# Optimization experiments

Hardware: AMD Instinct MI355X
Metric: run time of the kernel (lower is better)

Reference implementation:

```python
import jax, jax.numpy as jnp
import numpy as np
from jax import lax

T, B, D_IN, D_DAY, H, D_OUT = 64, 32, 4096, 256, 256, 942


def setup_inputs() -> dict:
    key = jax.random.key(0)
    ks = jax.random.split(key, 18)
    s = 0.05
    def rn(k, shape):
        return jax.random.normal(k, shape, jnp.float32) * s
    return {
        "x": jax.random.uniform(ks[0], (T, B, D_IN), jnp.float32),
        "W_emb": rn(ks[1], (D_DAY, D_IN)), "b_emb": rn(ks[2], (D_DAY,)),
        "Wih_f": rn(ks[3], (3 * H, D_DAY)), "Whh_f": rn(ks[4], (3 * H, H)),
        "bih_f": rn(ks[5], (3 * H,)), "bhh_f": rn(ks[6], (3 * H,)),
        "Wih_r": rn(ks[7], (3 * H, D_DAY)), "Whh_r": rn(ks[8], (3 * H, H)),
        "bih_r": rn(ks[9], (3 * H,)), "bhh_r": rn(ks[10], (3 * H,)),
        "attn_w": rn(ks[11], (2 * H,)), "attn_b": rn(ks[12], ()),
        "W_ao": rn(ks[13], (D_DAY, 4 * H)), "b_ao": rn(ks[14], (D_DAY,)),
        "W_o": rn(ks[15], (D_OUT, D_DAY)), "b_o": rn(ks[16], (D_OUT,)),
    }


def _gru_cell(xt, h, Wih, Whh, bih, bhh):
    # PyTorch nn.GRU cell math
    gi = xt @ Wih.T + bih          # [B, 3H]
    gh = h @ Whh.T + bhh           # [B, 3H]
    ir, iz, inn = jnp.split(gi, 3, axis=-1)
    hr, hz, hn = jnp.split(gh, 3, axis=-1)
    r = jax.nn.sigmoid(ir + hr)
    z = jax.nn.sigmoid(iz + hz)
    n = jnp.tanh(inn + r * hn)
    return (1.0 - z) * n + z * h


def _run_gru(seq, Wih, Whh, bih, bhh):
    # seq: [L, B, D] -> all hidden states [L, B, H], h0 = zeros
    h0 = jnp.zeros((seq.shape[1], H), seq.dtype)
    def step(h, xt):
        h2 = _gru_cell(xt, h, Wih, Whh, bih, bhh)
        return h2, h2
    return lax.scan(step, h0, seq)[1]


def reference(x, W_emb, b_emb, Wih_f, Whh_f, bih_f, bhh_f,
              Wih_r, Whh_r, bih_r, bhh_r, attn_w, attn_b,
              W_ao, b_ao, W_o, b_o):
    day_emb = jnp.einsum('tbi,di->tbd', x, W_emb) + b_emb       # [T,B,Dday]

    # Forward GRU over the prefix [:i+1] equals the first i+1 states of one full run.
    fwd = _run_gru(day_emb, Wih_f, Whh_f, bih_f, bhh_f)          # [T,B,H]

    # Reverse GRU is recomputed per timestep on the flipped prefix (O(T^2)).
    i_idx = jnp.arange(T)
    j_idx = jnp.arange(T)
    gather = jnp.clip(i_idx[:, None] - j_idx[None, :], 0)        # [T,T]
    rev_in = day_emb[gather]                                     # [T,T,B,Dday]; row i, step j = day_emb[i-j]
    rev = jax.vmap(lambda s: _run_gru(s, Wih_r, Whh_r, bih_r, bhh_r))(rev_in)  # [T,T,B,H]

    # Attention scores on concat(fwd, rev) without materializing the 2H concat:
    w_f, w_r = attn_w[:H], attn_w[H:]
    scores = (jnp.einsum('tbh,h->tb', fwd, w_f)[None, :, :]
              + jnp.einsum('itbh,h->itb', rev, w_r) + attn_b)    # [T(i),T(t),B]
    valid = j_idx[None, :] <= i_idx[:, None]                     # t <= i
    scores = jnp.where(valid[:, :, None], scores, -jnp.inf)
    alpha = jax.nn.softmax(scores, axis=1)                       # softmax over prefix time

    counts = (i_idx + 1).astype(day_emb.dtype)[:, None, None]    # mean over i+1 steps
    c_fwd = jnp.einsum('itb,tbh->ibh', alpha, fwd) / counts      # [T,B,H]
    c_rev = jnp.einsum('itb,itbh->ibh', alpha, rev) / counts     # [T,B,H]
    rev_last = rev[i_idx, i_idx]                                 # rnn_h[-1] reverse half, [T,B,H]

    h_t = jnp.concatenate([c_fwd, c_rev, fwd, rev_last], axis=-1)  # [T,B,4H]
    h_t_out = h_t @ W_ao.T + b_ao                                # [T,B,Dday]
    return jax.nn.sigmoid(h_t_out @ W_o.T + b_o)                 # [T,B,D_OUT]
```

## Files before the change

### kernel.cpp

```cpp
#include <hip/hip_runtime.h>
#include <hip/hip_bf16.h>


typedef __bf16 bf16x8 __attribute__((ext_vector_type(8)));
typedef __bf16 bf16x4 __attribute__((ext_vector_type(4)));
typedef float  f32x4  __attribute__((ext_vector_type(4)));
typedef int    int4v  __attribute__((ext_vector_type(4)));

static constexpr float NEG_L2E = -1.442695041f;
static constexpr float TWO_L2E =  2.885390082f;

static constexpr size_t OFF_PK_EMB = 0;
static constexpr size_t OFF_PK_IH  = 2097152;
static constexpr size_t OFF_WQ     = 2883584;
static constexpr size_t OFF_WSC    = 3276800;
static constexpr size_t OFF_PK_AO  = 3670016;
static constexpr size_t OFF_PK_O   = 4194304;
static constexpr size_t OFF_DAY    = 4685824;
static constexpr size_t OFF_GIT    = 5734400;
static constexpr size_t OFF_BC     = 12025856;
static constexpr size_t OFF_REV    = 18317312;
static constexpr size_t OFF_FWD    = 52396032;
static constexpr size_t OFF_HT     = 53444608;
static constexpr size_t OFF_TMP1   = 57638912;
static constexpr size_t OFF_XB     = OFF_REV;

__device__ __forceinline__ float sigf(float x) {
    return __builtin_amdgcn_rcpf(1.f + __expf(-x));
}

#define LDS_BARRIER() asm volatile("s_waitcnt lgkmcnt(0)\n\ts_barrier" ::: "memory")

__global__ __launch_bounds__(256) void pack_misc(
    const float* __restrict__ We,  const float* __restrict__ Wir, const float* __restrict__ Wif,
    const float* __restrict__ Wao, const float* __restrict__ Wo,  const float* __restrict__ x,
    const float* __restrict__ Whr, const float* __restrict__ Whf,
    const float* __restrict__ bih_r, const float* __restrict__ bih_f,
    const float* __restrict__ bhh_r, const float* __restrict__ bhh_f,
    __bf16* pe, __bf16* pi, __bf16* pao, __bf16* po, __bf16* xb,
    signed char* __restrict__ wq, float* __restrict__ wscale, float* __restrict__ bc)
{
    int b = blockIdx.x;
    if (b >= 5048) {
        int rowb = (b - 5048) * 4 + (threadIdx.x >> 6);
        int t = threadIdx.x & 63;
        int dir = (rowb >= 768) ? 1 : 0;
        int n = rowb - dir * 768;
        const float* src = (dir ? Whf : Whr) + (size_t)n * 256;
        float4 wv = ((const float4*)src)[t];
        float m = fmaxf(fmaxf(fabsf(wv.x), fabsf(wv.y)), fmaxf(fabsf(wv.z), fabsf(wv.w)));
#pragma unroll
        for (int off = 32; off > 0; off >>= 1) m = fmaxf(m, __shfl_xor(m, off));
        m = fmaxf(m, 1e-20f);
        float inv = 127.f / m;
        int q0 = (int)__builtin_rintf(wv.x * inv);
        int q1 = (int)__builtin_rintf(wv.y * inv);
        int q2 = (int)__builtin_rintf(wv.z * inv);
        int q3 = (int)__builtin_rintf(wv.w * inv);
        int pk = (q0 & 0xff) | ((q1 & 0xff) << 8) | ((q2 & 0xff) << 16) | ((q3 & 0xff) << 24);
        int dlane = (n & 15) | (((t >> 2) & 3) << 4);
        size_t byte = (size_t)dir * 196608 + ((size_t)(n >> 4) * 4 + (t >> 4)) * 1024
                    + (size_t)dlane * 16 + (t & 3) * 4;
        *(int*)(wq + byte) = pk;
        if (t == 0) {
            float gc = (n < 512) ? NEG_L2E : TWO_L2E;
            wscale[rowb] = m * (1.f / 16129.f) * gc;
            const float* bi = dir ? bih_f : bih_r;
            const float* bh = dir ? bhh_f : bhh_r;
            bc[rowb] = (n < 512) ? (bi[n] + bh[n]) * NEG_L2E : bi[n] * TWO_L2E;
        }
        return;
    }
    if (b >= 952) {
        size_t base = ((size_t)(b - 952) * 256 + threadIdx.x) * 8;
        float4 v0 = *(const float4*)(x + base);
        float4 v1 = *(const float4*)(x + base + 4);
        bf16x8 o;
        o[0]=(__bf16)v0.x; o[1]=(__bf16)v0.y; o[2]=(__bf16)v0.z; o[3]=(__bf16)v0.w;
        o[4]=(__bf16)v1.x; o[5]=(__bf16)v1.y; o[6]=(__bf16)v1.z; o[7]=(__bf16)v1.w;
        *(bf16x8*)(xb + base) = o;
        return;
    }
    const float* src; __bf16* dst; int Nsrc, k32l, b0; bool ih = false;
    if (b < 512)      { src = We;  dst = pe;          Nsrc = 256; k32l = 7; b0 = 0;   }
    else if (b < 608) { src = Wir; dst = pi;          Nsrc = 768; k32l = 3; b0 = 512; ih = true; }
    else if (b < 704) { src = Wif; dst = pi + 196608; Nsrc = 768; k32l = 3; b0 = 608; ih = true; }
    else if (b < 832) { src = Wao; dst = pao;         Nsrc = 256; k32l = 5; b0 = 704; }
    else              { src = Wo;  dst = po;          Nsrc = 942; k32l = 3; b0 = 832; }
    int t8   = (b - b0) * 256 + threadIdx.x;
    int lane = t8 & 63;
    int K32  = 1 << k32l;
    int K    = K32 << 5;
    int ks   = (t8 >> 6) & (K32 - 1);
    int nt   = t8 >> (6 + k32l);
    int n    = nt * 16 + (lane & 15);
    int k0   = ks * 32 + ((lane >> 4) << 3);
    bf16x8 o;
    if (n < Nsrc) {
        const float* sp = src + (size_t)n * K + k0;
        float4 v0 = *(const float4*)sp;
        float4 v1 = *(const float4*)(sp + 4);
        float s = ih ? ((n < 512) ? NEG_L2E : TWO_L2E) : 1.f;
        o[0]=(__bf16)(v0.x*s); o[1]=(__bf16)(v0.y*s); o[2]=(__bf16)(v0.z*s); o[3]=(__bf16)(v0.w*s);
        o[4]=(__bf16)(v1.x*s); o[5]=(__bf16)(v1.y*s); o[6]=(__bf16)(v1.z*s); o[7]=(__bf16)(v1.w*s);
    } else {
#pragma unroll
        for (int q = 0; q < 8; q++) o[q] = (__bf16)0.f;
    }
    *(bf16x8*)(dst + (size_t)t8 * 8) = o;
}

template<int MODE, int KDIM, int NTILES, int CSTRIDE, int NREAL>
__global__ __launch_bounds__(256) void gemm_k(
    const __bf16* __restrict__ Ap, const __bf16* __restrict__ Bp, void* __restrict__ Cp,
    const float* __restrict__ bias)
{
    __shared__ __align__(16) __bf16 As[32][88];
    const int tid = threadIdx.x;
    const int w = tid >> 6, lane = tid & 63, c = lane & 15, quad = lane >> 4;
    const int mb = blockIdx.x, nb = blockIdx.y;
    constexpr int K32 = KDIM / 32;
    constexpr int NK  = KDIM / 64;
    constexpr int NT_W = NTILES / 2;
    const int wrow = w & 1, ncol0 = (w >> 1) * NT_W;

    f32x4 acc[NT_W];
#pragma unroll
    for (int nt = 0; nt < NT_W; nt++) acc[nt] = (f32x4){0.f, 0.f, 0.f, 0.f};

    const int row = tid >> 3, kp = (tid & 7) * 8;
    uint4 pb;
    auto issue  = [&](int kb) { pb = *(const uint4*)(Ap + (size_t)(mb * 32 + row) * KDIM + kb * 64 + kp); };
    auto commit = [&]() { *(uint4*)&As[row][kp] = pb; };

    bf16x8 bcur[2][NT_W], bnxt[2][NT_W];
    auto loadB = [&](int kb, bf16x8 (&dst)[2][NT_W]) {
#pragma unroll
        for (int kk = 0; kk < 2; kk++)
#pragma unroll
            for (int nt = 0; nt < NT_W; nt++)
                dst[kk][nt] = *(const bf16x8*)(Bp +
                    ((size_t)((nb * NTILES + ncol0 + nt) * K32 + kb * 2 + kk) * 64 + lane) * 8);
    };

    issue(0);
    loadB(0, bcur);
    for (int kb = 0; kb < NK; kb++) {
        commit();
        __syncthreads();
        if (kb + 1 < NK) { issue(kb + 1); loadB(kb + 1, bnxt); }
#pragma unroll
        for (int kk = 0; kk < 2; kk++) {
            bf16x8 a = *(const bf16x8*)&As[wrow * 16 + c][kk * 32 + quad * 8];
#pragma unroll
            for (int nt = 0; nt < NT_W; nt++)
                acc[nt] = __builtin_amdgcn_mfma_f32_16x16x32_bf16(a, bcur[kk][nt], acc[nt], 0, 0, 0);
        }
        if (kb + 1 < NK) {
#pragma unroll
            for (int kk = 0; kk < 2; kk++)
#pragma unroll
                for (int nt = 0; nt < NT_W; nt++) bcur[kk][nt] = bnxt[kk][nt];
        }
        __syncthreads();
    }

#pragma unroll
    for (int nt = 0; nt < NT_W; nt++) {
        int n = nb * (NTILES * 16) + (ncol0 + nt) * 16 + c;
        float bv = (n < NREAL) ? bias[n] : 0.f;
#pragma unroll
        for (int r0 = 0; r0 < 4; r0++) {
            int m = mb * 32 + wrow * 16 + quad * 4 + r0;
            float v = acc[nt][r0] + bv;
            if constexpr (MODE == 0) ((__bf16*)Cp)[(size_t)m * CSTRIDE + n] = (__bf16)v;
            else { if (n < NREAL) ((float*)Cp)[(size_t)m * CSTRIDE + n] = sigf(v); }
        }
    }
}

__global__ __launch_bounds__(1024, 4) void gru_recurrent(
    const signed char* __restrict__ wq, const float* __restrict__ wscale,
    const float* __restrict__ bhh_r, const float* __restrict__ bhh_f,
    const __bf16* __restrict__ Gi,
    __bf16* __restrict__ revb, __bf16* __restrict__ fwdb)
{
    __shared__ __align__(16) signed char hbuf[2][4096];
    const int tid = threadIdx.x;
    const int w = tid >> 6, lane = tid & 63, c = lane & 15, quad = lane >> 4;
    const int bid = blockIdx.x;
    const bool isF = (bid < 2);
    const int ia = isF ? 63 : (63 - ((bid - 2) >> 1));
    const int b0 = (bid & 1) << 4;
    const int steps = ia + 1;
    const float* bhh = isF ? bhh_f : bhh_r;
    __bf16* outb = isF ? fwdb : (revb + ((size_t)(ia * (ia + 1) / 2)) * 8192);
    const int dirb = isF ? 768 : 0;

    const int4v* pw = (const int4v*)(wq + (isF ? 196608 : 0));
    int4v bw[3][4];
#pragma unroll
    for (int g = 0; g < 3; g++)
#pragma unroll
        for (int ks = 0; ks < 4; ks++)
            bw[g][ks] = pw[(size_t)((g * 16 + w) * 4 + ks) * 64 + lane];

    const int dq = (w << 4) + (quad << 2);
    f32x4 sc0 = *(const f32x4*)&wscale[dirb + dq];
    f32x4 sc1 = *(const f32x4*)&wscale[dirb + 256 + dq];
    f32x4 sc2 = *(const f32x4*)&wscale[dirb + 512 + dq];
    f32x4 bnv = *(const f32x4*)&bhh[512 + dq];
#pragma unroll
    for (int q = 0; q < 4; q++) bnv[q] *= TWO_L2E;

    float hreg[4] = {0.f, 0.f, 0.f, 0.f};
    ((int*)hbuf)[tid] = 0; ((int*)hbuf)[tid + 1024] = 0;
    __syncthreads();

    const __bf16* grow = Gi + (size_t)((isF ? 0 : ia) * 32 + b0 + c) * 1536 + dirb + dq;
    const long gstep = isF ? (32 * 1536) : -(32 * 1536);
    __bf16* go = outb + (size_t)(b0 + c) * 256 + dq;

    const int wr_off = (w >> 2) * 1024 + ((c + ((w & 3) << 4)) << 4) + (quad << 2);
    const int rd_off = lane << 4;

    bf16x4 gcur[3], gnxt[3];
#pragma unroll
    for (int g = 0; g < 3; g++) gcur[g] = *(const bf16x4*)(grow + g * 256);

    for (int j = 0; j < steps; j++) {
        const int rb = j & 1, wbuf = rb ^ 1;
        const bool more = (j + 1 < steps);

        if (more) {
            grow += gstep;
#pragma unroll
            for (int g = 0; g < 3; g++) gnxt[g] = *(const bf16x4*)(grow + g * 256);
        }

        int4v a0 = {0,0,0,0}, a1 = {0,0,0,0}, a2 = {0,0,0,0};
#pragma unroll
        for (int ks = 0; ks < 4; ks++) {
            int4v av = *(const int4v*)&hbuf[rb][ks * 1024 + rd_off];
            a0 = __builtin_amdgcn_mfma_i32_16x16x64_i8(bw[0][ks], av, a0, 0, 0, 0);
            a1 = __builtin_amdgcn_mfma_i32_16x16x64_i8(bw[1][ks], av, a1, 0, 0, 0);
            a2 = __builtin_amdgcn_mfma_i32_16x16x64_i8(bw[2][ks], av, a2, 0, 0, 0);
        }

        float f[4];
        bf16x4 hb;
#pragma unroll
        for (int r0 = 0; r0 < 4; r0++) {
            float er = __builtin_amdgcn_exp2f(fmaf((float)a0[r0], sc0[r0], (float)gcur[0][r0]));
            float rg = __builtin_amdgcn_rcpf(1.f + er);
            float ez = __builtin_amdgcn_exp2f(fmaf((float)a1[r0], sc1[r0], (float)gcur[1][r0]));
            float zg = __builtin_amdgcn_rcpf(1.f + ez);
            float narg = fmaf(rg, fmaf((float)a2[r0], sc2[r0], bnv[r0]), (float)gcur[2][r0]);
            float en = __builtin_amdgcn_exp2f(narg);
            float ng = fmaf(-2.f, __builtin_amdgcn_rcpf(1.f + en), 1.f);
            float h  = fmaf(zg, hreg[r0] - ng, ng);
            hreg[r0] = h;
            hb[r0] = (__bf16)h;
            f[r0] = fmaf(h, 127.f, 12582912.f);
        }
        unsigned lo = __builtin_amdgcn_perm(__float_as_uint(f[1]), __float_as_uint(f[0]), 0x00000400u);
        unsigned hi = __builtin_amdgcn_perm(__float_as_uint(f[3]), __float_as_uint(f[2]), 0x04000000u);
        int pk = (int)__builtin_amdgcn_perm(hi, lo, 0x07060100u);

        *(int*)&hbuf[wbuf][wr_off] = pk;
        *(bf16x4*)go = hb;
        go += 8192;
        LDS_BARRIER();
        if (more) {
#pragma unroll
            for (int g = 0; g < 3; g++) gcur[g] = gnxt[g];
        }
    }
}

__global__ __launch_bounds__(512) void attn_kernel(
    const __bf16* __restrict__ revb, const __bf16* __restrict__ fwdb,
    const float* __restrict__ attn_w, const float* __restrict__ attn_bp,
    __bf16* __restrict__ ht)
{
    const int tid = threadIdx.x;
    const int w = tid >> 6, lane = tid & 63;
    const int wid = blockIdx.x * 8 + w;
    const int i = wid >> 5, b = wid & 31;
    const int d0 = lane * 4;

    float wf[4], wr[4];
#pragma unroll
    for (int q = 0; q < 4; q++) { wf[q] = attn_w[d0 + q]; wr[q] = attn_w[256 + d0 + q]; }
    const float ab = attn_bp[0];
    const __bf16* rp = revb + ((size_t)(i * (i + 1) / 2)) * 8192 + (size_t)b * 256 + d0;
    const __bf16* fp = fwdb + (size_t)b * 256 + d0;

    float mx = -1e30f, l = 0.f;
    float cf[4] = {0,0,0,0}, cr[4] = {0,0,0,0};
    bf16x4 rn = *(const bf16x4*)rp, fn = *(const bf16x4*)fp;
    for (int t = 0; t <= i; t++) {
        bf16x4 rv4 = rn, fv4 = fn;
        if (t < i) {
            rn = *(const bf16x4*)(rp + (size_t)(t + 1) * 8192);
            fn = *(const bf16x4*)(fp + (size_t)(t + 1) * 8192);
        }
        float rv[4], fv[4], s = 0.f;
#pragma unroll
        for (int q = 0; q < 4; q++) {
            rv[q] = (float)rv4[q]; fv[q] = (float)fv4[q];
            s += rv[q] * wr[q] + fv[q] * wf[q];
        }
#pragma unroll
        for (int off = 32; off > 0; off >>= 1) s += __shfl_xor(s, off);
        s += ab;
        float mn = fmaxf(mx, s);
        float scl = __expf(mx - mn);
        float p  = __expf(s - mn);
        l = l * scl + p;
#pragma unroll
        for (int q = 0; q < 4; q++) { cf[q] = cf[q] * scl + p * fv[q]; cr[q] = cr[q] * scl + p * rv[q]; }
        mx = mn;
    }
    float inv = __builtin_amdgcn_rcpf(l * (float)(i + 1));
    __bf16* hp = ht + (size_t)(i * 32 + b) * 1024 + d0;
    const __bf16* fl = fp + (size_t)i * 8192;
    const __bf16* rl = rp + (size_t)i * 8192;
#pragma unroll
    for (int q = 0; q < 4; q++) {
        hp[q]       = (__bf16)(cf[q] * inv);
        hp[256 + q] = (__bf16)(cr[q] * inv);
        hp[512 + q] = fl[q];
        hp[768 + q] = rl[q];
    }
}

extern "C" void kernel_launch(void* const* d_in, const int* in_sizes, int n_in,
                              void* d_out, int out_size, void* d_ws, size_t ws_size,
                              hipStream_t stream) {
    const float* x      = (const float*)d_in[0];
    const float* W_emb  = (const float*)d_in[1];
    const float* b_emb  = (const float*)d_in[2];
    const float* Wih_f  = (const float*)d_in[3];
    const float* Whh_f  = (const float*)d_in[4];
    const float* bih_f  = (const float*)d_in[5];
    const float* bhh_f  = (const float*)d_in[6];
    const float* Wih_r  = (const float*)d_in[7];
    const float* Whh_r  = (const float*)d_in[8];
    const float* bih_r  = (const float*)d_in[9];
    const float* bhh_r  = (const float*)d_in[10];
    const float* attn_w = (const float*)d_in[11];
    const float* attn_b = (const float*)d_in[12];
    const float* W_ao   = (const float*)d_in[13];
    const float* b_ao   = (const float*)d_in[14];
    const float* W_o    = (const float*)d_in[15];
    const float* b_o    = (const float*)d_in[16];
    float* out = (float*)d_out;

    char* ws = (char*)d_ws;
    __bf16* pk_emb = (__bf16*)(ws + OFF_PK_EMB);
    __bf16* pk_ih  = (__bf16*)(ws + OFF_PK_IH);
    signed char* wq = (signed char*)(ws + OFF_WQ);
    float*  wsc    = (float*)(ws + OFF_WSC);
    __bf16* pk_ao  = (__bf16*)(ws + OFF_PK_AO);
    __bf16* pk_o   = (__bf16*)(ws + OFF_PK_O);
    __bf16* day    = (__bf16*)(ws + OFF_DAY);
    __bf16* Gi     = (__bf16*)(ws + OFF_GIT);
    float*  bc     = (float*)(ws + OFF_BC);
    __bf16* revb   = (__bf16*)(ws + OFF_REV);
    __bf16* fwdb   = (__bf16*)(ws + OFF_FWD);
    __bf16* ht     = (__bf16*)(ws + OFF_HT);
    __bf16* tmp1   = (__bf16*)(ws + OFF_TMP1);
    __bf16* xb     = (__bf16*)(ws + OFF_XB);

    pack_misc<<<5432, 256, 0, stream>>>(W_emb, Wih_r, Wih_f, W_ao, W_o, x,
                                        Whh_r, Whh_f, bih_r, bih_f, bhh_r, bhh_f,
                                        pk_emb, pk_ih, pk_ao, pk_o, xb, wq, wsc, bc);

    gemm_k<0, 4096, 4, 256, 256><<<dim3(64, 4), 256, 0, stream>>>(xb, pk_emb, day, b_emb);
    gemm_k<0, 256, 4, 1536, 1536><<<dim3(64, 24), 256, 0, stream>>>(day, pk_ih, Gi, bc);

    gru_recurrent<<<130, 1024, 0, stream>>>(wq, wsc, bhh_r, bhh_f, Gi, revb, fwdb);

    attn_kernel<<<256, 512, 0, stream>>>(revb, fwdb, attn_w, attn_b, ht);

    gemm_k<0, 1024, 4, 256, 256><<<dim3(64, 4), 256, 0, stream>>>(ht, pk_ao, tmp1, b_ao);
    gemm_k<1, 256, 4, 942, 942><<<dim3(64, 15), 256, 0, stream>>>(tmp1, pk_o, out, b_o);
}
```

Before: 330.1 us.

## Halve GRU recurrent block size with two M-tiles per wave

The recurrent GRU kernel now runs 512 threads per block instead of 1024. Each wave computes two 16-row output tiles per gate, doubling its register-resident int8 weights and the number of MFMAs per step. The next-step Gi prefetch is moved after the MFMAs and gate math, replacing the previous double-buffered prefetch registers. This is meant to cut barrier cost per step and to increase independent MFMA work within each wave, at the cost of higher register pressure and more serial work per wave on the critical recurrent path.

```diff
diff --git a/kernel.cpp b/kernel.cpp
--- a/kernel.cpp
+++ b/kernel.cpp
@@ -179,7 +179,33 @@
     }
 }
 
-__global__ __launch_bounds__(1024, 4) void gru_recurrent(
+__device__ __forceinline__ void gru_cell4(
+    const int4v a0, const int4v a1, const int4v a2,
+    const f32x4 sc0, const f32x4 sc1, const f32x4 sc2, const f32x4 bnv,
+    const bf16x4 g0, const bf16x4 g1, const bf16x4 g2,
+    float* hreg, int* pk, bf16x4* hb)
+{
+    float f[4];
+#pragma unroll
+    for (int r = 0; r < 4; r++) {
+        float er = __builtin_amdgcn_exp2f(fmaf((float)a0[r], sc0[r], (float)g0[r]));
+        float rg = __builtin_amdgcn_rcpf(1.f + er);
+        float ez = __builtin_amdgcn_exp2f(fmaf((float)a1[r], sc1[r], (float)g1[r]));
+        float zg = __builtin_amdgcn_rcpf(1.f + ez);
+        float narg = fmaf(rg, fmaf((float)a2[r], sc2[r], bnv[r]), (float)g2[r]);
+        float en = __builtin_amdgcn_exp2f(narg);
+        float ng = fmaf(-2.f, __builtin_amdgcn_rcpf(1.f + en), 1.f);
+        float h  = fmaf(zg, hreg[r] - ng, ng);
+        hreg[r] = h;
+        (*hb)[r] = (__bf16)h;
+        f[r] = fmaf(h, 127.f, 12582912.f);
+    }
+    unsigned lo = __builtin_amdgcn_perm(__float_as_uint(f[1]), __float_as_uint(f[0]), 0x00000400u);
+    unsigned hi = __builtin_amdgcn_perm(__float_as_uint(f[3]), __float_as_uint(f[2]), 0x04000000u);
+    *pk = (int)__builtin_amdgcn_perm(hi, lo, 0x07060100u);
+}
+
+__global__ __launch_bounds__(512, 2) void gru_recurrent(
     const signed char* __restrict__ wq, const float* __restrict__ wscale,
     const float* __restrict__ bhh_r, const float* __restrict__ bhh_f,
     const __bf16* __restrict__ Gi,
@@ -198,83 +224,91 @@
     const int dirb = isF ? 768 : 0;
 
     const int4v* pw = (const int4v*)(wq + (isF ? 196608 : 0));
-    int4v bw[3][4];
+    int4v bw[3][2][4];
 #pragma unroll
     for (int g = 0; g < 3; g++)
 #pragma unroll
-        for (int ks = 0; ks < 4; ks++)
-            bw[g][ks] = pw[(size_t)((g * 16 + w) * 4 + ks) * 64 + lane];
-
-    const int dq = (w << 4) + (quad << 2);
-    f32x4 sc0 = *(const f32x4*)&wscale[dirb + dq];
-    f32x4 sc1 = *(const f32x4*)&wscale[dirb + 256 + dq];
-    f32x4 sc2 = *(const f32x4*)&wscale[dirb + 512 + dq];
-    f32x4 bnv = *(const f32x4*)&bhh[512 + dq];
-#pragma unroll
-    for (int q = 0; q < 4; q++) bnv[q] *= TWO_L2E;
-
-    float hreg[4] = {0.f, 0.f, 0.f, 0.f};
-    ((int*)hbuf)[tid] = 0; ((int*)hbuf)[tid + 1024] = 0;
+        for (int mt = 0; mt < 2; mt++)
+#pragma unroll
+            for (int ks = 0; ks < 4; ks++)
+                bw[g][mt][ks] = pw[(size_t)((g * 16 + 2 * w + mt) * 4 + ks) * 64 + lane];
+
+    const int d0 = (w << 5) + (quad << 2);
+    const int d1 = d0 + 16;
+    f32x4 sc[3][2], bnv[2];
+#pragma unroll
+    for (int g = 0; g < 3; g++)
+#pragma unroll
+        for (int mt = 0; mt < 2; mt++)
+            sc[g][mt] = *(const f32x4*)&wscale[dirb + g * 256 + d0 + 16 * mt];
+#pragma unroll
+    for (int mt = 0; mt < 2; mt++) {
+        bnv[mt] = *(const f32x4*)&bhh[512 + d0 + 16 * mt];
+#pragma unroll
+        for (int q = 0; q < 4; q++) bnv[mt][q] *= TWO_L2E;
+    }
+
+    float hreg[8] = {0.f, 0.f, 0.f, 0.f, 0.f, 0.f, 0.f, 0.f};
+    ((int*)hbuf)[tid]        = 0; ((int*)hbuf)[tid + 512]  = 0;
+    ((int*)hbuf)[tid + 1024] = 0; ((int*)hbuf)[tid + 1536] = 0;
     __syncthreads();
 
-    const __bf16* grow = Gi + (size_t)((isF ? 0 : ia) * 32 + b0 + c) * 1536 + dirb + dq;
+    const __bf16* grow = Gi + (size_t)((isF ? 0 : ia) * 32 + b0 + c) * 1536 + dirb;
     const long gstep = isF ? (32 * 1536) : -(32 * 1536);
-    __bf16* go = outb + (size_t)(b0 + c) * 256 + dq;
-
-    const int wr_off = (w >> 2) * 1024 + ((c + ((w & 3) << 4)) << 4) + (quad << 2);
+    __bf16* go = outb + (size_t)(b0 + c) * 256 + d0;
+
+    const int wr0 = ((d0 >> 6) << 10) + ((c | (((d0 >> 4) & 3) << 4)) << 4) + (d0 & 15);
+    const int wr1 = ((d1 >> 6) << 10) + ((c | (((d1 >> 4) & 3) << 4)) << 4) + (d1 & 15);
     const int rd_off = lane << 4;
 
-    bf16x4 gcur[3], gnxt[3];
-#pragma unroll
-    for (int g = 0; g < 3; g++) gcur[g] = *(const bf16x4*)(grow + g * 256);
+    bf16x4 gc[3][2];
+#pragma unroll
+    for (int g = 0; g < 3; g++)
+#pragma unroll
+        for (int mt = 0; mt < 2; mt++)
+            gc[g][mt] = *(const bf16x4*)(grow + g * 256 + d0 + 16 * mt);
 
     for (int j = 0; j < steps; j++) {
         const int rb = j & 1, wbuf = rb ^ 1;
         const bool more = (j + 1 < steps);
 
+        int4v acc[3][2];
+#pragma unroll
+        for (int g = 0; g < 3; g++)
+#pragma unroll
+            for (int mt = 0; mt < 2; mt++) acc[g][mt] = (int4v){0, 0, 0, 0};
+#pragma unroll
+        for (int ks = 0; ks < 4; ks++) {
+            int4v av = *(const int4v*)&hbuf[rb][ks * 1024 + rd_off];
+#pragma unroll
+            for (int g = 0; g < 3; g++) {
+                acc[g][0] = __builtin_amdgcn_mfma_i32_16x16x64_i8(bw[g][0][ks], av, acc[g][0], 0, 0, 0);
+                acc[g][1] = __builtin_amdgcn_mfma_i32_16x16x64_i8(bw[g][1][ks], av, acc[g][1], 0, 0, 0);
+            }
+        }
+
+        int pk0, pk1; bf16x4 hb0, hb1;
+        gru_cell4(acc[0][0], acc[1][0], acc[2][0], sc[0][0], sc[1][0], sc[2][0], bnv[0],
+                  gc[0][0], gc[1][0], gc[2][0], &hreg[0], &pk0, &hb0);
+        gru_cell4(acc[0][1], acc[1][1], acc[2][1], sc[0][1], sc[1][1], sc[2][1], bnv[1],
+                  gc[0][1], gc[1][1], gc[2][1], &hreg[4], &pk1, &hb1);
+
+        *(int*)&hbuf[wbuf][wr0] = pk0;
+        *(int*)&hbuf[wbuf][wr1] = pk1;
+
         if (more) {
             grow += gstep;
 #pragma unroll
-            for (int g = 0; g < 3; g++) gnxt[g] = *(const bf16x4*)(grow + g * 256);
-        }
-
-        int4v a0 = {0,0,0,0}, a1 = {0,0,0,0}, a2 = {0,0,0,0};
-#pragma unroll
-        for (int ks = 0; ks < 4; ks++) {
-            int4v av = *(const int4v*)&hbuf[rb][ks * 1024 + rd_off];
-            a0 = __builtin_amdgcn_mfma_i32_16x16x64_i8(bw[0][ks], av, a0, 0, 0, 0);
-            a1 = __builtin_amdgcn_mfma_i32_16x16x64_i8(bw[1][ks], av, a1, 0, 0, 0);
-            a2 = __builtin_amdgcn_mfma_i32_16x16x64_i8(bw[2][ks], av, a2, 0, 0, 0);
-        }
-
-        float f[4];
-        bf16x4 hb;
-#pragma unroll
-        for (int r0 = 0; r0 < 4; r0++) {
-            float er = __builtin_amdgcn_exp2f(fmaf((float)a0[r0], sc0[r0], (float)gcur[0][r0]));
-            float rg = __builtin_amdgcn_rcpf(1.f + er);
-            float ez = __builtin_amdgcn_exp2f(fmaf((float)a1[r0], sc1[r0], (float)gcur[1][r0]));
-            float zg = __builtin_amdgcn_rcpf(1.f + ez);
-            float narg = fmaf(rg, fmaf((float)a2[r0], sc2[r0], bnv[r0]), (float)gcur[2][r0]);
-            float en = __builtin_amdgcn_exp2f(narg);
-            float ng = fmaf(-2.f, __builtin_amdgcn_rcpf(1.f + en), 1.f);
-            float h  = fmaf(zg, hreg[r0] - ng, ng);
-            hreg[r0] = h;
-            hb[r0] = (__bf16)h;
-            f[r0] = fmaf(h, 127.f, 12582912.f);
-        }
-        unsigned lo = __builtin_amdgcn_perm(__float_as_uint(f[1]), __float_as_uint(f[0]), 0x00000400u);
-        unsigned hi = __builtin_amdgcn_perm(__float_as_uint(f[3]), __float_as_uint(f[2]), 0x04000000u);
-        int pk = (int)__builtin_amdgcn_perm(hi, lo, 0x07060100u);
-
-        *(int*)&hbuf[wbuf][wr_off] = pk;
-        *(bf16x4*)go = hb;
+            for (int g = 0; g < 3; g++)
+#pragma unroll
+                for (int mt = 0; mt < 2; mt++)
+                    gc[g][mt] = *(const bf16x4*)(grow + g * 256 + d0 + 16 * mt);
+        }
+
+        *(bf16x4*)go = hb0;
+        *(bf16x4*)(go + 16) = hb1;
         go += 8192;
         LDS_BARRIER();
-        if (more) {
-#pragma unroll
-            for (int g = 0; g < 3; g++) gcur[g] = gnxt[g];
-        }
     }
 }
 
@@ -380,7 +414,7 @@
     gemm_k<0, 4096, 4, 256, 256><<<dim3(64, 4), 256, 0, stream>>>(xb, pk_emb, day, b_emb);
     gemm_k<0, 256, 4, 1536, 1536><<<dim3(64, 24), 256, 0, stream>>>(day, pk_ih, Gi, bc);
 
-    gru_recurrent<<<130, 1024, 0, stream>>>(wq, wsc, bhh_r, bhh_f, Gi, revb, fwdb);
+    gru_recurrent<<<130, 512, 0, stream>>>(wq, wsc, bhh_r, bhh_f, Gi, revb, fwdb);
 
     attn_kernel<<<256, 512, 0, stream>>>(revb, fwdb, attn_w, attn_b, ht);
 
```

After: 309.0 us. -6.4%, faster.
